# Performance work log

Measured on AMD Instinct MI355X. Metric: run time of the kernel, lower is better.

## Reference

```python
import jax, jax.numpy as jnp
import numpy as np

HALF_FEATURE_NUMEL = 49152  # 12 pieces * 64 squares * 64 king buckets
INTER_DIM = 768             # factorizer collapses king bucket: i % 768


def setup_inputs() -> dict:
    key = jax.random.key(0)
    k1, k2, k3, k4 = jax.random.split(key, 4)
    N = 16384
    nnz = N * 32  # ~32 active features per position
    batch_idx = jnp.sort(jax.random.randint(k1, (nnz,), 0, N, dtype=jnp.int64 if jax.config.read('jax_enable_x64') else jnp.int32))
    active_idx = jax.random.randint(k2, (nnz,), 0, HALF_FEATURE_NUMEL)
    values = jax.random.uniform(k3, (nnz,), dtype=jnp.float32)
    # factorization table self.f = [func(i) for i in range(half_feature_numel)]
    f_table = jnp.arange(HALF_FEATURE_NUMEL) % INTER_DIM
    weights = jax.random.normal(k4, (INTER_DIM, 256), dtype=jnp.float32) * 0.01
    return {"batch_idx": batch_idx, "active_idx": active_idx, "values": values,
            "f_table": f_table, "weights": weights, "N": N}


def reference(batch_idx, active_idx, values, f_table, weights, N):
    # gather: remap active feature ids through factorization table
    factored = f_table[active_idx]                      # [nnz]
    inter_dim = weights.shape[0]
    # scatter-sum duplicates into dense [N, inter_dim] (== sparse COO .to_dense())
    x = jnp.zeros((N, inter_dim), dtype=values.dtype)
    x = x.at[batch_idx, factored].add(values)
    # dense matmul with factored weights
    return x @ weights                                  # [N, output_dim]
```

## Files before the change

### kernel.cpp

```cpp
#include <hip/hip_runtime.h>


#define OUT_COLS 256
#define WAVES_PER_BLOCK 4
#define BLOCK_THREADS (WAVES_PER_BLOCK * 64)

__global__ __launch_bounds__(256)
void build_kernel(const int* __restrict__ batch_idx,
                  const int* __restrict__ active_idx,
                  const float* __restrict__ values,
                  const int* __restrict__ f_table,
                  int* __restrict__ offsets,
                  int2* __restrict__ pairs,
                  int nnz, int N)
{
    const int k = blockIdx.x * blockDim.x + threadIdx.x;
    if (k >= nnz) return;
    const int r  = batch_idx[k];
    const int rp = (k == 0) ? -1 : batch_idx[k - 1];
    for (int row = rp + 1; row <= r; ++row) offsets[row] = k;
    if (k == nnz - 1)
        for (int row = r + 1; row <= N; ++row) offsets[row] = nnz;
    if (pairs)
        pairs[k] = make_int2(f_table[active_idx[k]], __float_as_int(values[k]));
}

__global__ __launch_bounds__(BLOCK_THREADS, 8)
void gemm_kernel(const int* __restrict__ offsets,
                 const int2* __restrict__ pairs,
                 const float* __restrict__ weights,
                 float* __restrict__ out, int N)
{
    const int lane = threadIdx.x & 63;
    const int row  = blockIdx.x * WAVES_PER_BLOCK + (threadIdx.x >> 6);
    if (row >= N) return;

    const int start = __builtin_amdgcn_readfirstlane(offsets[row]);
    const int end   = __builtin_amdgcn_readfirstlane(offsets[row + 1]);

    float4 acc = make_float4(0.f, 0.f, 0.f, 0.f);
    const float* __restrict__ wbase = weights + (lane << 2);

    int k = start;
    for (; k + 8 <= end; k += 8) {
        int2 p[8];
#pragma unroll
        for (int j = 0; j < 8; ++j) p[j] = pairs[k + j];
        float4 w[8];
#pragma unroll
        for (int j = 0; j < 8; ++j)
            w[j] = *(const float4*)(wbase + p[j].x * OUT_COLS);
#pragma unroll
        for (int j = 0; j < 8; ++j) {
            const float v = __int_as_float(p[j].y);
            acc.x = fmaf(v, w[j].x, acc.x);
            acc.y = fmaf(v, w[j].y, acc.y);
            acc.z = fmaf(v, w[j].z, acc.z);
            acc.w = fmaf(v, w[j].w, acc.w);
        }
    }
    for (; k < end; ++k) {
        const int2 p = pairs[k];
        const float v = __int_as_float(p.y);
        const float4 w = *(const float4*)(wbase + p.x * OUT_COLS);
        acc.x = fmaf(v, w.x, acc.x);
        acc.y = fmaf(v, w.y, acc.y);
        acc.z = fmaf(v, w.z, acc.z);
        acc.w = fmaf(v, w.w, acc.w);
    }

    *(float4*)(out + row * OUT_COLS + (lane << 2)) = acc;
}

__global__ __launch_bounds__(BLOCK_THREADS, 8)
void fallback_kernel(const int* __restrict__ batch_idx,
                     const int* __restrict__ active_idx,
                     const float* __restrict__ values,
                     const int* __restrict__ f_table,
                     const float* __restrict__ weights,
                     float* __restrict__ out,
                     int nnz, int N)
{
    const int wave = threadIdx.x >> 6;
    const int lane = threadIdx.x & 63;
    const int row  = blockIdx.x * WAVES_PER_BLOCK + wave;
    if (row >= N) return;

    int lo1 = 0, hi1 = nnz, lo2 = 0, hi2 = nnz;
    while ((lo1 < hi1) | (lo2 < hi2)) {
        if (lo1 < hi1) { int m = (lo1 + hi1) >> 1; if (batch_idx[m] < row) lo1 = m + 1; else hi1 = m; }
        if (lo2 < hi2) { int m = (lo2 + hi2) >> 1; if (batch_idx[m] < row + 1) lo2 = m + 1; else hi2 = m; }
    }
    float4 acc = make_float4(0.f, 0.f, 0.f, 0.f);
    const float* __restrict__ wcol = weights + (lane << 2);
    for (int base = lo1; base < lo2; base += 64) {
        const int cnt = min(lo2 - base, 64);
        float v_l = 0.f; int f_l = 0;
        if (lane < cnt) { const int k = base + lane; v_l = values[k]; f_l = f_table[active_idx[k]]; }
        for (int j = 0; j < cnt; ++j) {
            const float v = __shfl(v_l, j);
            const int   f = __shfl(f_l, j);
            const float4 w = *(const float4*)(wcol + f * OUT_COLS);
            acc.x = fmaf(v, w.x, acc.x);
            acc.y = fmaf(v, w.y, acc.y);
            acc.z = fmaf(v, w.z, acc.z);
            acc.w = fmaf(v, w.w, acc.w);
        }
    }
    *(float4*)(out + row * OUT_COLS + (lane << 2)) = acc;
}

extern "C" void kernel_launch(void* const* d_in, const int* in_sizes, int n_in,
                              void* d_out, int out_size, void* d_ws, size_t ws_size,
                              hipStream_t stream) {
    const int*   batch_idx  = (const int*)d_in[0];
    const int*   active_idx = (const int*)d_in[1];
    const float* values     = (const float*)d_in[2];
    const int*   f_table    = (const int*)d_in[3];
    const float* weights    = (const float*)d_in[4];
    float*       out        = (float*)d_out;

    const int nnz = in_sizes[0];
    const int N   = out_size / OUT_COLS;

    const size_t off_bytes   = (size_t)(N + 1) * sizeof(int);
    const size_t pairs_off   = (off_bytes + 15) & ~(size_t)15;
    const size_t need_pairs  = pairs_off + (size_t)nnz * sizeof(int2);

    const int grid_rows = (N + WAVES_PER_BLOCK - 1) / WAVES_PER_BLOCK;

    if (ws_size >= need_pairs) {
        int*  offsets = (int*)d_ws;
        int2* pairs   = (int2*)((char*)d_ws + pairs_off);
        const int grid_nnz = (nnz + 255) / 256;
        build_kernel<<<grid_nnz, 256, 0, stream>>>(batch_idx, active_idx, values,
                                                   f_table, offsets, pairs, nnz, N);
        gemm_kernel<<<grid_rows, BLOCK_THREADS, 0, stream>>>(offsets, pairs, weights, out, N);
    } else {
        fallback_kernel<<<grid_rows, BLOCK_THREADS, 0, stream>>>(
            batch_idx, active_idx, values, f_table, weights, out, nnz, N);
    }
}
```

Before: 96.24 us.

## Split each row's nonzeros across four waves and reduce partials via LDS

The gather-GEMM kernel now assigns one block per output row, and its four waves interleave 8-element chunks of the row's nonzeros. Each wave keeps its own partial accumulator, and the partials are summed through shared memory after a barrier. This shortens the serial per-wave dependency chain and exposes more memory-level parallelism per row. The cost is four times as many blocks, an LDS reduction with a barrier, and idle waves when a row has few nonzeros (about 32 on average).

```diff
diff --git a/kernel.cpp b/kernel.cpp
--- a/kernel.cpp
+++ b/kernel.cpp
@@ -2,8 +2,7 @@
 
 
 #define OUT_COLS 256
-#define WAVES_PER_BLOCK 4
-#define BLOCK_THREADS (WAVES_PER_BLOCK * 64)
+#define BLOCK_THREADS 256
 
 __global__ __launch_bounds__(256)
 void build_kernel(const int* __restrict__ batch_idx,
@@ -21,8 +20,7 @@
     for (int row = rp + 1; row <= r; ++row) offsets[row] = k;
     if (k == nnz - 1)
         for (int row = r + 1; row <= N; ++row) offsets[row] = nnz;
-    if (pairs)
-        pairs[k] = make_int2(f_table[active_idx[k]], __float_as_int(values[k]));
+    pairs[k] = make_int2(f_table[active_idx[k]], __float_as_int(values[k]));
 }
 
 __global__ __launch_bounds__(BLOCK_THREADS, 8)
@@ -31,9 +29,11 @@
                  const float* __restrict__ weights,
                  float* __restrict__ out, int N)
 {
+    __shared__ float4 partial[3][64];
+
     const int lane = threadIdx.x & 63;
-    const int row  = blockIdx.x * WAVES_PER_BLOCK + (threadIdx.x >> 6);
-    if (row >= N) return;
+    const int wave = threadIdx.x >> 6;
+    const int row  = blockIdx.x;
 
     const int start = __builtin_amdgcn_readfirstlane(offsets[row]);
     const int end   = __builtin_amdgcn_readfirstlane(offsets[row + 1]);
@@ -41,38 +41,52 @@
     float4 acc = make_float4(0.f, 0.f, 0.f, 0.f);
     const float* __restrict__ wbase = weights + (lane << 2);
 
-    int k = start;
-    for (; k + 8 <= end; k += 8) {
-        int2 p[8];
+    for (int k0 = start + wave * 8; k0 < end; k0 += 32) {
+        const int cnt = min(end - k0, 8);
+        if (cnt == 8) {
+            int2 p[8];
 #pragma unroll
-        for (int j = 0; j < 8; ++j) p[j] = pairs[k + j];
-        float4 w[8];
+            for (int j = 0; j < 8; ++j) p[j] = pairs[k0 + j];
+            float4 w[8];
 #pragma unroll
-        for (int j = 0; j < 8; ++j)
-            w[j] = *(const float4*)(wbase + p[j].x * OUT_COLS);
+            for (int j = 0; j < 8; ++j)
+                w[j] = *(const float4*)(wbase + p[j].x * OUT_COLS);
 #pragma unroll
-        for (int j = 0; j < 8; ++j) {
-            const float v = __int_as_float(p[j].y);
-            acc.x = fmaf(v, w[j].x, acc.x);
-            acc.y = fmaf(v, w[j].y, acc.y);
-            acc.z = fmaf(v, w[j].z, acc.z);
-            acc.w = fmaf(v, w[j].w, acc.w);
+            for (int j = 0; j < 8; ++j) {
+                const float v = __int_as_float(p[j].y);
+                acc.x = fmaf(v, w[j].x, acc.x);
+                acc.y = fmaf(v, w[j].y, acc.y);
+                acc.z = fmaf(v, w[j].z, acc.z);
+                acc.w = fmaf(v, w[j].w, acc.w);
+            }
+        } else {
+            for (int j = 0; j < cnt; ++j) {
+                const int2 p = pairs[k0 + j];
+                const float v = __int_as_float(p.y);
+                const float4 w = *(const float4*)(wbase + p.x * OUT_COLS);
+                acc.x = fmaf(v, w.x, acc.x);
+                acc.y = fmaf(v, w.y, acc.y);
+                acc.z = fmaf(v, w.z, acc.z);
+                acc.w = fmaf(v, w.w, acc.w);
+            }
         }
     }
-    for (; k < end; ++k) {
-        const int2 p = pairs[k];
-        const float v = __int_as_float(p.y);
-        const float4 w = *(const float4*)(wbase + p.x * OUT_COLS);
-        acc.x = fmaf(v, w.x, acc.x);
-        acc.y = fmaf(v, w.y, acc.y);
-        acc.z = fmaf(v, w.z, acc.z);
-        acc.w = fmaf(v, w.w, acc.w);
+
+    if (wave != 0) partial[wave - 1][lane] = acc;
+    __syncthreads();
+    if (wave == 0) {
+        const float4 p0 = partial[0][lane];
+        const float4 p1 = partial[1][lane];
+        const float4 p2 = partial[2][lane];
+        acc.x += p0.x + p1.x + p2.x;
+        acc.y += p0.y + p1.y + p2.y;
+        acc.z += p0.z + p1.z + p2.z;
+        acc.w += p0.w + p1.w + p2.w;
+        *(float4*)(out + row * OUT_COLS + (lane << 2)) = acc;
     }
-
-    *(float4*)(out + row * OUT_COLS + (lane << 2)) = acc;
 }
 
-__global__ __launch_bounds__(BLOCK_THREADS, 8)
+__global__ __launch_bounds__(256, 8)
 void fallback_kernel(const int* __restrict__ batch_idx,
                      const int* __restrict__ active_idx,
                      const float* __restrict__ values,
@@ -83,7 +97,7 @@
 {
     const int wave = threadIdx.x >> 6;
     const int lane = threadIdx.x & 63;
-    const int row  = blockIdx.x * WAVES_PER_BLOCK + wave;
+    const int row  = blockIdx.x * 4 + wave;
     if (row >= N) return;
 
     int lo1 = 0, hi1 = nnz, lo2 = 0, hi2 = nnz;
@@ -123,21 +137,19 @@
     const int nnz = in_sizes[0];
     const int N   = out_size / OUT_COLS;
 
-    const size_t off_bytes   = (size_t)(N + 1) * sizeof(int);
-    const size_t pairs_off   = (off_bytes + 15) & ~(size_t)15;
-    const size_t need_pairs  = pairs_off + (size_t)nnz * sizeof(int2);
+    const size_t off_bytes  = (size_t)(N + 1) * sizeof(int);
+    const size_t pairs_off  = (off_bytes + 15) & ~(size_t)15;
+    const size_t need_bytes = pairs_off + (size_t)nnz * sizeof(int2);
 
-    const int grid_rows = (N + WAVES_PER_BLOCK - 1) / WAVES_PER_BLOCK;
-
-    if (ws_size >= need_pairs) {
+    if (ws_size >= need_bytes) {
         int*  offsets = (int*)d_ws;
         int2* pairs   = (int2*)((char*)d_ws + pairs_off);
         const int grid_nnz = (nnz + 255) / 256;
         build_kernel<<<grid_nnz, 256, 0, stream>>>(batch_idx, active_idx, values,
                                                    f_table, offsets, pairs, nnz, N);
-        gemm_kernel<<<grid_rows, BLOCK_THREADS, 0, stream>>>(offsets, pairs, weights, out, N);
+        gemm_kernel<<<N, BLOCK_THREADS, 0, stream>>>(offsets, pairs, weights, out, N);
     } else {
-        fallback_kernel<<<grid_rows, BLOCK_THREADS, 0, stream>>>(
+        fallback_kernel<<<(N + 3) / 4, 256, 0, stream>>>(
             batch_idx, active_idx, values, f_table, weights, out, nnz, N);
     }
 }
```

Result: slower. 105.9 us (+10.1%).
